# Kernel optimization log

Measured on AMD Instinct MI355X. Metric: run time of the kernel, lower is better.

## Reference

```python
import jax, jax.numpy as jnp
import numpy as np

BOS = 1
MAX_LEN = 20


def _lstm_cell(x, h, c, Wih, Whh, bih, bhh):
    # torch.nn.LSTMCell gate order: i, f, g, o
    g = x @ Wih.T + h @ Whh.T + bih + bhh
    i, f, gg, o = jnp.split(g, 4, axis=-1)
    c = jax.nn.sigmoid(f) * c + jax.nn.sigmoid(i) * jnp.tanh(gg)
    h = jax.nn.sigmoid(o) * jnp.tanh(c)
    return h, c


def setup_inputs() -> dict:
    key = jax.random.key(0)
    ks = jax.random.split(key, 12)
    B, K, D = 512, 36, 2048
    A, H, Em, V = 512, 512, 300, 10000
    s = 0.02
    rn = lambda k, shape, sc=s: sc * jax.random.normal(k, shape, dtype=jnp.float32)
    return {
        'feats': jax.random.normal(ks[0], (B, K, D), dtype=jnp.float32),
        'Wp': rn(ks[1], (A, D)), 'bp': jnp.zeros((A,), jnp.float32),
        'E': rn(ks[2], (V, Em), 0.1).at[0].set(0.0),  # padding_idx = 0
        'Wih1': rn(ks[3], (4 * H, Em + A)), 'Whh1': rn(ks[4], (4 * H, H)),
        'bih1': jnp.zeros((4 * H,), jnp.float32), 'bhh1': jnp.zeros((4 * H,), jnp.float32),
        'Wih2': rn(ks[5], (4 * H, H + A)), 'Whh2': rn(ks[6], (4 * H, H)),
        'bih2': jnp.zeros((4 * H,), jnp.float32), 'bhh2': jnp.zeros((4 * H,), jnp.float32),
        'Wa1': rn(ks[7], (A, H + A)), 'ba1': jnp.zeros((A,), jnp.float32),
        'wa2': rn(ks[8], (1, A)), 'ba2': jnp.zeros((1,), jnp.float32),
        'Wo': rn(ks[9], (V, H)), 'bo': jnp.zeros((V,), jnp.float32),
    }


def reference(feats, Wp, bp, E, Wih1, Whh1, bih1, bhh1, Wih2, Whh2, bih2, bhh2,
              Wa1, ba1, wa2, ba2, Wo, bo):
    B, K, D = feats.shape
    H = Whh1.shape[1]
    f_att = feats @ Wp.T + bp                      # [B, K, A]
    f_mean = f_att.mean(axis=1)                    # [B, A]
    # attn Linear over concat([h1, f_att]): split columns, precompute f_att term
    Wa1_h, Wa1_f = Wa1[:, :H], Wa1[:, H:]
    att_f = f_att @ Wa1_f.T + ba1                  # [B, K, A]
    x0 = jnp.broadcast_to(E[BOS], (B, E.shape[1]))
    z = jnp.zeros((B, H), jnp.float32)
    carry0 = (x0, z, z, z, z)

    def step(carry, _):
        x, h1, c1, h2, c2 = carry
        h1, c1 = _lstm_cell(jnp.concatenate([x, f_mean], axis=-1), h1, c1,
                            Wih1, Whh1, bih1, bhh1)
        pre = jnp.tanh(att_f + (h1 @ Wa1_h.T)[:, None, :])   # [B, K, A]
        e = pre @ wa2[0] + ba2[0]                            # [B, K]
        alpha = jax.nn.softmax(e, axis=-1)
        ctx = jnp.einsum('bk,bka->ba', alpha, f_att)         # [B, A]
        h2, c2 = _lstm_cell(jnp.concatenate([h1, ctx], axis=-1), h2, c2,
                            Wih2, Whh2, bih2, bhh2)
        logit = h2 @ Wo.T + bo                               # [B, V]  (dropout is identity in eval)
        nxt = jnp.argmax(logit, axis=-1)
        return (E[nxt], h1, c1, h2, c2), nxt

    _, ids = jax.lax.scan(step, carry0, None, length=MAX_LEN - 1)
    return ids.T  # [B, MAX_LEN-1], matches torch.stack(out_ids, 1)
```

## Files before the change

kernel.cpp:

```cpp
#include <hip/hip_runtime.h>
#include <math.h>
#include <stdint.h>

constexpr int Bsz = 512, Kf = 36, Dd = 2048, Aa = 512, Hh = 512, Em = 300;
constexpr int Vv = 10000, TSTEPS = 19, BOS = 1;
constexpr int K1 = 832;
constexpr int K2 = 1536;
constexpr int VvP = 10112;
constexpr int NTL = VvP / 64;
constexpr float SPLIT_S  = 2048.0f;
constexpr float SPLIT_IS = 1.0f / 2048.0f;

#define CDIV(a,b) (((a)+(b)-1)/(b))

typedef _Float16 f16x8 __attribute__((ext_vector_type(8)));
typedef float    f32x4 __attribute__((ext_vector_type(4)));

typedef const unsigned int GU __attribute__((address_space(1)));
typedef unsigned int       LU __attribute__((address_space(3)));

__device__ __forceinline__ void gload16(const void* g, void* l) {
    __builtin_amdgcn_global_load_lds((GU*)g, (LU*)l, 16, 0, 0);
}

template<int N> __device__ __forceinline__ void wait_vm() {
    if constexpr (N == 0)       asm volatile("s_waitcnt vmcnt(0)" ::: "memory");
    else if constexpr (N == 4)  asm volatile("s_waitcnt vmcnt(4)" ::: "memory");
    else if constexpr (N == 6)  asm volatile("s_waitcnt vmcnt(6)" ::: "memory");
    else if constexpr (N == 8)  asm volatile("s_waitcnt vmcnt(8)" ::: "memory");
    else if constexpr (N == 12) asm volatile("s_waitcnt vmcnt(12)" ::: "memory");
    else if constexpr (N == 16) asm volatile("s_waitcnt vmcnt(16)" ::: "memory");
    else static_assert(N == 0, "unsupported vmcnt literal");
}
#define WAIT_LGKM asm volatile("s_waitcnt lgkmcnt(0)" ::: "memory")
#define SB0 __builtin_amdgcn_sched_barrier(0)
#define BAR __builtin_amdgcn_s_barrier()

__device__ __forceinline__ float sigm(float v) { return 1.0f / (1.0f + expf(-v)); }

__device__ __forceinline__ void wsplit(_Float16* __restrict__ hi, _Float16* __restrict__ lo,
                                       size_t idx, float v) {
    _Float16 h = (_Float16)v;
    hi[idx] = h;
    lo[idx] = (_Float16)((v - (float)h) * SPLIT_S);
}


template<int BM, int BN, int BK, int DEPTH, int WVM, bool AF32, bool SWZ, int OCC, int EPI, int PAD>
__global__ __launch_bounds__(256, OCC)
void gemm_sp(const float* __restrict__ Af,
             const _Float16* __restrict__ Ahi, const _Float16* __restrict__ Alo, int lda,
             const _Float16* __restrict__ Bhi, const _Float16* __restrict__ Blo, int ldb,
             float* __restrict__ C, int ldc, int N, int K,
             const float* __restrict__ bias1, const float* __restrict__ bias2,
             const float* __restrict__ addC, int gxn,
             float* __restrict__ cbuf,
             _Float16* __restrict__ d1h, _Float16* __restrict__ d1l, int ld1, int off1,
             _Float16* __restrict__ d2h, _Float16* __restrict__ d2l, int ld2, int off2,
             float* __restrict__ candV, int* __restrict__ candI, int ntl)
{
    static_assert(EPI != 2 || WVM == 4, "LSTM epilogue needs 4x1 wave grid");
    constexpr int WVN = 4 / WVM;
    constexpr int WM = BM / WVM, WN = BN / WVN;
    constexpr int MF = WM / 16, NF = WN / 16;
    constexpr int PA  = BK / 8;
    constexpr int PSA = BM * 8 + PAD;
    constexpr int PSB = BN * 8 + PAD;
    static_assert(PAD == 0 || (BM >= 64 && BN >= 64), "PAD needs wave-aligned planes");
    constexpr int SZA = PA * PSA, SZB = PA * PSB;
    constexpr int OAH = 0, OAL = SZA, OBH = 2 * SZA, OBL = 2 * SZA + SZB;
    constexpr int BUF = 2 * SZA + 2 * SZB;
    constexpr int NCHA = BM * BK / 2048;
    constexpr int NCHB = BN * BK / 2048;
    static_assert(NCHA >= 1 && NCHB >= 1, "tile too small for 256-thread stage");
    constexpr int LW = 2 * NCHA + 2 * NCHB;
    static_assert((DEPTH & (DEPTH - 1)) == 0, "DEPTH pow2");
    static_assert(!AF32 || DEPTH == 2, "AF32 path is double-buffered");
    __shared__ _Float16 sm[DEPTH * BUF];

    int mt, nt;
    if constexpr (SWZ) {
        const int nwg = gridDim.x;
        const int cpx = nwg >> 3;
        const int orig = blockIdx.x;
        const int lid = (orig & 7) * cpx + (orig >> 3);
        nt = lid % gxn; mt = lid / gxn;
    } else {
        nt = blockIdx.x; mt = blockIdx.y;
    }
    const int m0 = mt * BM, n0 = nt * BN;

    const int t    = threadIdx.x;
    const int lane = t & 63;
    const int w    = t >> 6;
    const int wr   = w / WVN, wc = w % WVN;
    const int l15  = lane & 15, l4 = lane >> 4;

    f32x4 acch[MF][NF];
    f32x4 accm[MF][NF];
    #pragma unroll
    for (int m = 0; m < MF; ++m)
        #pragma unroll
        for (int n = 0; n < NF; ++n) {
            acch[m][n] = (f32x4){0.f, 0.f, 0.f, 0.f};
            accm[m][n] = (f32x4){0.f, 0.f, 0.f, 0.f};
        }

    const int nkt = K / BK;

    auto stageB = [&](int bufo, int kt) {
        #pragma unroll
        for (int i = 0; i < NCHB; ++i) {
            const int q  = i * 256 + t;
            const int p  = q / BN, r = q % BN;
            const int qw = i * 256 + (t & ~63);
            const int pu = qw / BN, ru = qw % BN;
            const size_t goff = (size_t)(n0 + r) * ldb + kt * BK + p * 8;
            gload16(Bhi + goff, &sm[bufo + OBH + pu * PSB + ru * 8]);
            gload16(Blo + goff, &sm[bufo + OBL + pu * PSB + ru * 8]);
        }
    };
    auto stageA16 = [&](int bufo, int kt) {
        #pragma unroll
        for (int i = 0; i < NCHA; ++i) {
            const int q  = i * 256 + t;
            const int p  = q / BM, r = q % BM;
            const int qw = i * 256 + (t & ~63);
            const int pu = qw / BM, ru = qw % BM;
            const size_t goff = (size_t)(m0 + r) * lda + kt * BK + p * 8;
            gload16(Ahi + goff, &sm[bufo + OAH + pu * PSA + ru * 8]);
            gload16(Alo + goff, &sm[bufo + OAL + pu * PSA + ru * 8]);
        }
    };
    auto issueA = [&](float4 (&rd)[NCHA][2], int kt) {
        #pragma unroll
        for (int i = 0; i < NCHA; ++i) {
            const int q = i * 256 + t;
            const int p = q / BM, r = q % BM;
            const float* src = Af + (size_t)(m0 + r) * lda + kt * BK + p * 8;
            rd[i][0] = *(const float4*)src;
            rd[i][1] = *(const float4*)(src + 4);
        }
    };
    auto writeA = [&](int bufo, float4 (&rd)[NCHA][2]) {
        #pragma unroll
        for (int i = 0; i < NCHA; ++i) {
            const int q = i * 256 + t;
            const int p = q / BM, r = q % BM;
            const float f[8] = {rd[i][0].x, rd[i][0].y, rd[i][0].z, rd[i][0].w,
                                rd[i][1].x, rd[i][1].y, rd[i][1].z, rd[i][1].w};
            f16x8 hi, lo;
            #pragma unroll
            for (int j = 0; j < 8; ++j) {
                _Float16 h = (_Float16)f[j];
                hi[j] = h;
                lo[j] = (_Float16)((f[j] - (float)h) * SPLIT_S);
            }
            *(f16x8*)&sm[bufo + OAH + p * PSA + r * 8] = hi;
            *(f16x8*)&sm[bufo + OAL + p * PSA + r * 8] = lo;
        }
    };
    auto compute = [&](int bufo) {
        #pragma unroll
        for (int s = 0; s < BK / 32; ++s) {
            f16x8 ah[MF], al[MF], bh[NF], bl[NF];
            const int pl = s * 4 + l4;
            #pragma unroll
            for (int m = 0; m < MF; ++m) {
                const int row = wr * WM + m * 16 + l15;
                ah[m] = *(const f16x8*)&sm[bufo + OAH + pl * PSA + row * 8];
                al[m] = *(const f16x8*)&sm[bufo + OAL + pl * PSA + row * 8];
            }
            #pragma unroll
            for (int n = 0; n < NF; ++n) {
                const int row = wc * WN + n * 16 + l15;
                bh[n] = *(const f16x8*)&sm[bufo + OBH + pl * PSB + row * 8];
                bl[n] = *(const f16x8*)&sm[bufo + OBL + pl * PSB + row * 8];
            }
            #pragma unroll
            for (int m = 0; m < MF; ++m)
                #pragma unroll
                for (int n = 0; n < NF; ++n) {
                    acch[m][n] = __builtin_amdgcn_mfma_f32_16x16x32_f16(ah[m], bh[n], acch[m][n], 0, 0, 0);
                    accm[m][n] = __builtin_amdgcn_mfma_f32_16x16x32_f16(ah[m], bl[n], accm[m][n], 0, 0, 0);
                    accm[m][n] = __builtin_amdgcn_mfma_f32_16x16x32_f16(al[m], bh[n], accm[m][n], 0, 0, 0);
                }
        }
    };

    if constexpr (AF32) {
        float4 rA[NCHA][2], rB[NCHA][2];
        issueA(rA, 0); stageB(0, 0);
        for (int kt = 0; kt < nkt; kt += 2) {
            issueA(rB, kt + 1); stageB(BUF, kt + 1);
            wait_vm<LW>(); SB0;
            writeA(0, rA);
            WAIT_LGKM; SB0;
            BAR; SB0;
            compute(0);
            SB0; WAIT_LGKM; BAR; SB0;
            if (kt + 2 < nkt) { issueA(rA, kt + 2); stageB(0, kt + 2); wait_vm<LW>(); }
            else              { wait_vm<0>(); }
            SB0;
            writeA(BUF, rB);
            WAIT_LGKM; SB0;
            BAR; SB0;
            compute(BUF);
            SB0; WAIT_LGKM; BAR; SB0;
        }
    } else {
        #pragma unroll
        for (int d = 0; d < DEPTH - 1; ++d) { stageA16(d * BUF, d); stageB(d * BUF, d); }
        for (int kt = 0; kt < nkt; ++kt) {
            const int bc = (kt & (DEPTH - 1)) * BUF;
            if (kt + DEPTH - 1 < nkt) {
                const int bn = ((kt + DEPTH - 1) & (DEPTH - 1)) * BUF;
                stageA16(bn, kt + DEPTH - 1); stageB(bn, kt + DEPTH - 1);
                wait_vm<(DEPTH - 1) * LW>();
            } else {
                const int rem = nkt - 1 - kt;
                if constexpr (DEPTH >= 4) {
                    if (rem >= 2)      wait_vm<2 * LW>();
                    else if (rem == 1) wait_vm<LW>();
                    else               wait_vm<0>();
                } else {
                    if (rem >= 1) wait_vm<LW>(); else wait_vm<0>();
                }
            }
            SB0;
            BAR; SB0;
            compute(bc);
            SB0; WAIT_LGKM; BAR; SB0;
        }
    }

    if constexpr (EPI == 0 || EPI == 1) {
        #pragma unroll
        for (int m = 0; m < MF; ++m) {
            const int rowb = m0 + wr * WM + m * 16 + l4 * 4;
            #pragma unroll
            for (int n = 0; n < NF; ++n) {
                const int col = n0 + wc * WN + n * 16 + l15;
                if (col < N) {
                    float bb = 0.f;
                    if (bias1) {
                        int bx = col;
                        if constexpr (EPI == 1)
                            bx = ((col & 63) >> 4) * 512 + ((col >> 6) << 4) + (col & 15);
                        bb += bias1[bx];
                        if (bias2) bb += bias2[bx];
                    }
                    #pragma unroll
                    for (int r = 0; r < 4; ++r) {
                        const size_t idx = (size_t)(rowb + r) * ldc + col;
                        float v = acch[m][n][r] + accm[m][n][r] * SPLIT_IS + bb;
                        if (addC) v += addC[idx];
                        C[idx] = v;
                    }
                }
            }
        }
    } else if constexpr (EPI == 2) {
        const int hh = (n0 >> 2) + l15;
        #pragma unroll
        for (int r = 0; r < 4; ++r) {
            const int row = m0 + wr * 16 + l4 * 4 + r;
            float v[4];
            #pragma unroll
            for (int n = 0; n < 4; ++n) {
                const int col = n0 + n * 16 + l15;
                float bb = 0.f;
                if (bias1) {
                    const int bx = ((col & 63) >> 4) * 512 + ((col >> 6) << 4) + (col & 15);
                    bb = bias1[bx] + bias2[bx];
                }
                float x = acch[0][n][r] + accm[0][n][r] * SPLIT_IS + bb;
                if (addC) x += addC[(size_t)row * ldc + col];
                v[n] = x;
            }
            const float cold = cbuf[(size_t)row * Hh + hh];
            const float cv = sigm(v[1]) * cold + sigm(v[0]) * tanhf(v[2]);
            cbuf[(size_t)row * Hh + hh] = cv;
            const float hv = sigm(v[3]) * tanhf(cv);
            wsplit(d1h, d1l, (size_t)row * ld1 + off1 + hh, hv);
            if (d2h) wsplit(d2h, d2l, (size_t)row * ld2 + off2 + hh, hv);
        }
    } else {
        float* sEv = reinterpret_cast<float*>(&sm[0]);
        int*   sEi = reinterpret_cast<int*>(&sm[0]) + 2 * BM;
        float bv[MF][4];
        int   bix[MF][4];
        #pragma unroll
        for (int m = 0; m < MF; ++m)
            #pragma unroll
            for (int r = 0; r < 4; ++r) { bv[m][r] = -INFINITY; bix[m][r] = 0x7fffffff; }
        #pragma unroll
        for (int m = 0; m < MF; ++m)
            #pragma unroll
            for (int r = 0; r < 4; ++r)
                #pragma unroll
                for (int n = 0; n < NF; ++n) {
                    const int col = n0 + wc * WN + n * 16 + l15;
                    if (col < N) {
                        const float x = acch[m][n][r] + accm[m][n][r] * SPLIT_IS + bias1[col];
                        if (x > bv[m][r]) { bv[m][r] = x; bix[m][r] = col; }
                    }
                }
        #pragma unroll
        for (int mask = 1; mask < 16; mask <<= 1) {
            #pragma unroll
            for (int m = 0; m < MF; ++m)
                #pragma unroll
                for (int r = 0; r < 4; ++r) {
                    const float ov = __shfl_xor(bv[m][r], mask);
                    const int   oi = __shfl_xor(bix[m][r], mask);
                    if (ov > bv[m][r] || (ov == bv[m][r] && oi < bix[m][r])) {
                        bv[m][r] = ov; bix[m][r] = oi;
                    }
                }
        }
        __syncthreads();
        if (l15 == 0) {
            #pragma unroll
            for (int m = 0; m < MF; ++m)
                #pragma unroll
                for (int r = 0; r < 4; ++r) {
                    const int rl = wr * WM + m * 16 + l4 * 4 + r;
                    sEv[wc * BM + rl] = bv[m][r];
                    sEi[wc * BM + rl] = bix[m][r];
                }
        }
        __syncthreads();
        if (t < BM) {
            float v0 = sEv[t]; int i0 = sEi[t];
            const float v1 = sEv[BM + t]; const int i1 = sEi[BM + t];
            if (v1 > v0 || (v1 == v0 && i1 < i0)) { v0 = v1; i0 = i1; }
            candV[(size_t)(m0 + t) * ntl + nt] = v0;
            candI[(size_t)(m0 + t) * ntl + nt] = i0;
        }
    }
}

__global__ __launch_bounds__(256)
void split_convert(const float* __restrict__ src, int srcld, int validR,
                   _Float16* __restrict__ dhi, _Float16* __restrict__ dlo,
                   int dstld, int coloff, int R, int C, int gperm)
{
    const int total = R * C;
    for (int i = blockIdx.x * 256 + threadIdx.x; i < total; i += gridDim.x * 256) {
        const int r = i / C, c = i % C;
        int dr = r;
        if (gperm) {
            const int gate = r >> 9, h = r & 511;
            dr = ((h >> 4) << 6) + (gate << 4) + (h & 15);
        }
        const float v = (r < validR) ? src[(size_t)r * srcld + c] : 0.f;
        wsplit(dhi, dlo, (size_t)dr * dstld + coloff + c, v);
    }
}

__global__ __launch_bounds__(256)
void init_kernel(_Float16* __restrict__ a1h0, _Float16* __restrict__ a1l0,
                 _Float16* __restrict__ a1h1, _Float16* __restrict__ a1l1,
                 _Float16* __restrict__ a2h0, _Float16* __restrict__ a2l0,
                 _Float16* __restrict__ a2h1, _Float16* __restrict__ a2l1,
                 float* __restrict__ c1, float* __restrict__ c2,
                 const float* __restrict__ E)
{
    const int idx = blockIdx.x * 256 + threadIdx.x;
    if (idx < Bsz * K1) {
        const int col = idx % K1;
        const float v = (col < Em) ? E[(size_t)BOS * Em + col] : 0.f;
        wsplit(a1h0, a1l0, idx, v);
        wsplit(a1h1, a1l1, idx, 0.f);
    }
    if (idx < Bsz * K2) {
        wsplit(a2h0, a2l0, idx, 0.f);
        wsplit(a2h1, a2l1, idx, 0.f);
    }
    if (idx < Bsz * Hh) { c1[idx] = 0.f; c2[idx] = 0.f; }
}

__global__ __launch_bounds__(256)
void fmean_kernel(const float* __restrict__ f_att, float* __restrict__ f_mean,
                  _Float16* __restrict__ fmh, _Float16* __restrict__ fml)
{
    const int b = blockIdx.x;
    for (int a = threadIdx.x; a < Aa; a += 256) {
        float s = 0.f;
        for (int k = 0; k < Kf; ++k) s += f_att[((size_t)b * Kf + k) * Aa + a];
        const float v = s * (1.0f / 36.0f);
        f_mean[(size_t)b * Aa + a] = v;
        wsplit(fmh, fml, (size_t)b * Aa + a, v);
    }
}

__global__ __launch_bounds__(256)
void attn_fused(const float* __restrict__ att_f, const float* __restrict__ q,
                const float* __restrict__ wa2, const float* __restrict__ ba2,
                const float* __restrict__ f_att,
                _Float16* __restrict__ a2h, _Float16* __restrict__ a2l)
{
    const int b = blockIdx.x, tid = threadIdx.x;
    const int w = tid >> 6, lane = tid & 63;
    __shared__ float se[Kf];
    __shared__ float wk[Kf];
    const float* pq = q + (size_t)b * Aa;
    for (int k = w; k < Kf; k += 4) {
        const float* pf = att_f + ((size_t)b * Kf + k) * Aa;
        float s = 0.f;
        #pragma unroll
        for (int j = 0; j < Aa; j += 64) {
            const int a = j + lane;
            s += tanhf(pf[a] + pq[a]) * wa2[a];
        }
        #pragma unroll
        for (int off = 32; off; off >>= 1) s += __shfl_down(s, off);
        if (lane == 0) se[k] = s + ba2[0];
    }
    __syncthreads();
    if (tid < Kf) {
        float mx = -INFINITY;
        for (int k = 0; k < Kf; ++k) mx = fmaxf(mx, se[k]);
        float ssum = 0.f;
        for (int k = 0; k < Kf; ++k) ssum += expf(se[k] - mx);
        wk[tid] = expf(se[tid] - mx) / ssum;
    }
    __syncthreads();
    for (int a = tid; a < Aa; a += 256) {
        float acc = 0.f;
        for (int k = 0; k < Kf; ++k)
            acc = fmaf(wk[k], f_att[((size_t)b * Kf + k) * Aa + a], acc);
        wsplit(a2h, a2l, (size_t)b * K2 + Hh + a, acc);
    }
}

__global__ __launch_bounds__(256)
void argmax_embed_kernel(const float* __restrict__ candV, const int* __restrict__ candI,
                         const float* __restrict__ E,
                         _Float16* __restrict__ a1h, _Float16* __restrict__ a1l,
                         int* __restrict__ out, int t, int ntl)
{
    const int b = blockIdx.x;
    const int tid = threadIdx.x;
    __shared__ float sv[256];
    __shared__ int   si[256];
    float bvv = -INFINITY; int bii = 0x7fffffff;
    if (tid < ntl) { bvv = candV[(size_t)b * ntl + tid]; bii = candI[(size_t)b * ntl + tid]; }
    sv[tid] = bvv; si[tid] = bii;
    __syncthreads();
    for (int s = 128; s > 0; s >>= 1) {
        if (tid < s) {
            const float v2 = sv[tid + s];
            const int   i2 = si[tid + s];
            if (v2 > sv[tid] || (v2 == sv[tid] && i2 < si[tid])) { sv[tid] = v2; si[tid] = i2; }
        }
        __syncthreads();
    }
    const int idx = si[0];
    if (tid == 0) out[(size_t)b * TSTEPS + t] = idx;
    for (int d = tid; d < Em; d += 256)
        wsplit(a1h, a1l, (size_t)b * K1 + d, E[(size_t)idx * Em + d]);
}

static inline void conv(hipStream_t s, const float* src, int srcld, int validR,
                        _Float16* dhi, _Float16* dlo, int dstld, int coloff,
                        int R, int C, int gperm)
{
    int blocks = CDIV(R * C, 256); if (blocks > 2048) blocks = 2048;
    split_convert<<<dim3(blocks), dim3(256), 0, s>>>(src, srcld, validR, dhi, dlo,
                                                     dstld, coloff, R, C, gperm);
}

extern "C" void kernel_launch(void* const* d_in, const int* in_sizes, int n_in,
                              void* d_out, int out_size, void* d_ws, size_t ws_size,
                              hipStream_t stream)
{
    const float* feats = (const float*)d_in[0];
    const float* Wp    = (const float*)d_in[1];
    const float* bp    = (const float*)d_in[2];
    const float* E     = (const float*)d_in[3];
    const float* Wih1  = (const float*)d_in[4];
    const float* Whh1  = (const float*)d_in[5];
    const float* bih1  = (const float*)d_in[6];
    const float* bhh1  = (const float*)d_in[7];
    const float* Wih2  = (const float*)d_in[8];
    const float* Whh2  = (const float*)d_in[9];
    const float* bih2  = (const float*)d_in[10];
    const float* bhh2  = (const float*)d_in[11];
    const float* Wa1   = (const float*)d_in[12];
    const float* ba1   = (const float*)d_in[13];
    const float* wa2   = (const float*)d_in[14];
    const float* ba2   = (const float*)d_in[15];
    const float* Wo    = (const float*)d_in[16];
    const float* bo    = (const float*)d_in[17];
    int* out = (int*)d_out;
    (void)in_sizes; (void)n_in; (void)out_size; (void)ws_size;

    uint8_t* w = (uint8_t*)d_ws;
    size_t off = 0;
    auto alloc = [&](size_t bytes) { void* p = w + off; off = (off + bytes + 255) & ~(size_t)255; return p; };

    float*     f_att  = (float*)alloc(18432ull * 512 * 4);
    float*     att_f  = (float*)alloc(18432ull * 512 * 4);
    float*     f_mean = (float*)alloc(512ull * 512 * 4);
    _Float16*  fmh    = (_Float16*)alloc(512ull * 512 * 2);
    _Float16*  fml    = (_Float16*)alloc(512ull * 512 * 2);
    _Float16*  wph    = (_Float16*)alloc(512ull * 2048 * 2);
    _Float16*  wpl    = (_Float16*)alloc(512ull * 2048 * 2);
    _Float16*  w1ph   = (_Float16*)alloc(2048ull * K1 * 2);
    _Float16*  w1pl   = (_Float16*)alloc(2048ull * K1 * 2);
    _Float16*  w1ch   = (_Float16*)alloc(2048ull * 512 * 2);
    _Float16*  w1cl   = (_Float16*)alloc(2048ull * 512 * 2);
    _Float16*  w2ph   = (_Float16*)alloc(2048ull * K2 * 2);
    _Float16*  w2pl   = (_Float16*)alloc(2048ull * K2 * 2);
    _Float16*  wahh   = (_Float16*)alloc(512ull * 512 * 2);
    _Float16*  wahl   = (_Float16*)alloc(512ull * 512 * 2);
    _Float16*  wafh   = (_Float16*)alloc(512ull * 512 * 2);
    _Float16*  wafl   = (_Float16*)alloc(512ull * 512 * 2);
    _Float16*  woh    = (_Float16*)alloc((size_t)VvP * 512 * 2);
    _Float16*  wol    = (_Float16*)alloc((size_t)VvP * 512 * 2);
    float*     g1c    = (float*)alloc(512ull * 2048 * 4);
    _Float16*  a1h[2] = {(_Float16*)alloc(512ull * K1 * 2), (_Float16*)alloc(512ull * K1 * 2)};
    _Float16*  a1l[2] = {(_Float16*)alloc(512ull * K1 * 2), (_Float16*)alloc(512ull * K1 * 2)};
    _Float16*  a2h[2] = {(_Float16*)alloc(512ull * K2 * 2), (_Float16*)alloc(512ull * K2 * 2)};
    _Float16*  a2l[2] = {(_Float16*)alloc(512ull * K2 * 2), (_Float16*)alloc(512ull * K2 * 2)};
    float*     c1     = (float*)alloc(512ull * 512 * 4);
    float*     c2     = (float*)alloc(512ull * 512 * 4);
    float*     qbuf   = (float*)alloc(512ull * 512 * 4);
    float*     candV  = (float*)alloc(512ull * NTL * 4);
    int*       candI  = (int*)alloc(512ull * NTL * 4);

    conv(stream, Wp,        Dd,      512,  wph,  wpl,  2048, 0,    512,  2048, 0);
    conv(stream, Wih1,      Em + Aa, 2048, w1ph, w1pl, K1,   0,    2048, Em,   1);
    conv(stream, Whh1,      Hh,      2048, w1ph, w1pl, K1,   Em,   2048, 512,  1);
    conv(stream, Wih1,      Em + Aa, 0,    w1ph, w1pl, K1,   812,  2048, 20,   0);
    conv(stream, Wih1 + Em, Em + Aa, 2048, w1ch, w1cl, 512,  0,    2048, 512,  1);
    conv(stream, Wih2,      Hh + Aa, 2048, w2ph, w2pl, K2,   0,    2048, 1024, 1);
    conv(stream, Whh2,      Hh,      2048, w2ph, w2pl, K2,   1024, 2048, 512,  1);
    conv(stream, Wa1,       Hh + Aa, 512,  wahh, wahl, 512,  0,    512,  512,  0);
    conv(stream, Wa1 + Hh,  Hh + Aa, 512,  wafh, wafl, 512,  0,    512,  512,  0);
    conv(stream, Wo,        Hh,      Vv,   woh,  wol,  512,  0,    VvP,  512,  0);

    init_kernel<<<dim3(CDIV(Bsz * K2, 256)), dim3(256), 0, stream>>>(
        a1h[0], a1l[0], a1h[1], a1l[1], a2h[0], a2l[0], a2h[1], a2l[1], c1, c2, E);

    gemm_sp<128, 64, 32, 2, 2, true, true, 2, 0, 8><<<dim3(1152), 256, 0, stream>>>(
        feats, nullptr, nullptr, Dd, wph, wpl, 2048, f_att, 512, 512, 2048,
        bp, nullptr, nullptr, 8,
        nullptr, nullptr, nullptr, 0, 0, nullptr, nullptr, 0, 0, nullptr, nullptr, 0);
    fmean_kernel<<<dim3(Bsz), dim3(256), 0, stream>>>(f_att, f_mean, fmh, fml);
    gemm_sp<64, 64, 64, 2, 2, false, false, 1, 1, 8><<<dim3(32, 8), 256, 0, stream>>>(
        nullptr, fmh, fml, 512, w1ch, w1cl, 512, g1c, 2048, 2048, 512,
        bih1, bhh1, nullptr, 0,
        nullptr, nullptr, nullptr, 0, 0, nullptr, nullptr, 0, 0, nullptr, nullptr, 0);
    gemm_sp<128, 64, 32, 2, 2, true, true, 2, 0, 8><<<dim3(1152), 256, 0, stream>>>(
        f_att, nullptr, nullptr, 512, wafh, wafl, 512, att_f, 512, 512, 512,
        ba1, nullptr, nullptr, 8,
        nullptr, nullptr, nullptr, 0, 0, nullptr, nullptr, 0, 0, nullptr, nullptr, 0);

    for (int t = 0; t < TSTEPS; ++t) {
        const int cur = t & 1, nxt = cur ^ 1;
        gemm_sp<64, 64, 32, 2, 4, false, false, 3, 2, 8><<<dim3(32, 8), 256, 0, stream>>>(
            nullptr, a1h[cur], a1l[cur], K1, w1ph, w1pl, K1, nullptr, 2048, 2048, K1,
            nullptr, nullptr, g1c, 0,
            c1, a2h[cur], a2l[cur], K2, 0, a1h[nxt], a1l[nxt], K1, Em,
            nullptr, nullptr, 0);
        gemm_sp<64, 64, 64, 2, 2, false, false, 1, 0, 8><<<dim3(8, 8), 256, 0, stream>>>(
            nullptr, a2h[cur], a2l[cur], K2, wahh, wahl, 512, qbuf, 512, 512, 512,
            nullptr, nullptr, nullptr, 0,
            nullptr, nullptr, nullptr, 0, 0, nullptr, nullptr, 0, 0, nullptr, nullptr, 0);
        attn_fused<<<dim3(Bsz), dim3(256), 0, stream>>>(
            att_f, qbuf, wa2, ba2, f_att, a2h[cur], a2l[cur]);
        gemm_sp<64, 64, 32, 2, 4, false, false, 3, 2, 8><<<dim3(32, 8), 256, 0, stream>>>(
            nullptr, a2h[cur], a2l[cur], K2, w2ph, w2pl, K2, nullptr, 2048, 2048, K2,
            bih2, bhh2, nullptr, 0,
            c2, a2h[nxt], a2l[nxt], K2, 1024, nullptr, nullptr, 0, 0,
            nullptr, nullptr, 0);
        gemm_sp<64, 64, 64, 2, 2, false, false, 1, 3, 8><<<dim3(NTL, 8), 256, 0, stream>>>(
            nullptr, a2h[nxt] + 1024, a2l[nxt] + 1024, K2, woh, wol, 512, nullptr, 0, Vv, 512,
            bo, nullptr, nullptr, 0,
            nullptr, nullptr, nullptr, 0, 0, nullptr, nullptr, 0, 0, candV, candI, NTL);
        argmax_embed_kernel<<<dim3(Bsz), dim3(256), 0, stream>>>(
            candV, candI, E, a1h[nxt], a1l[nxt], out, t, NTL);
    }
}
```

Measured before the change: 3.542 ms.

## Split fp32-A GEMM into dedicated 512-thread kernel and raise LSTM GEMM BK to 64

```diff
diff --git a/kernel.cpp b/kernel.cpp
--- a/kernel.cpp
+++ b/kernel.cpp
@@ -25,11 +25,9 @@
 
 template<int N> __device__ __forceinline__ void wait_vm() {
     if constexpr (N == 0)       asm volatile("s_waitcnt vmcnt(0)" ::: "memory");
-    else if constexpr (N == 4)  asm volatile("s_waitcnt vmcnt(4)" ::: "memory");
+    else if constexpr (N == 3)  asm volatile("s_waitcnt vmcnt(3)" ::: "memory");
     else if constexpr (N == 6)  asm volatile("s_waitcnt vmcnt(6)" ::: "memory");
     else if constexpr (N == 8)  asm volatile("s_waitcnt vmcnt(8)" ::: "memory");
-    else if constexpr (N == 12) asm volatile("s_waitcnt vmcnt(12)" ::: "memory");
-    else if constexpr (N == 16) asm volatile("s_waitcnt vmcnt(16)" ::: "memory");
     else static_assert(N == 0, "unsupported vmcnt literal");
 }
 #define WAIT_LGKM asm volatile("s_waitcnt lgkmcnt(0)" ::: "memory")
@@ -46,14 +44,13 @@
 }
 
 
-template<int BM, int BN, int BK, int DEPTH, int WVM, bool AF32, bool SWZ, int OCC, int EPI, int PAD>
+template<int BM, int BN, int BK, int WVM, int OCC, int EPI>
 __global__ __launch_bounds__(256, OCC)
-void gemm_sp(const float* __restrict__ Af,
-             const _Float16* __restrict__ Ahi, const _Float16* __restrict__ Alo, int lda,
+void gemm_sp(const _Float16* __restrict__ Ahi, const _Float16* __restrict__ Alo, int lda,
              const _Float16* __restrict__ Bhi, const _Float16* __restrict__ Blo, int ldb,
              float* __restrict__ C, int ldc, int N, int K,
              const float* __restrict__ bias1, const float* __restrict__ bias2,
-             const float* __restrict__ addC, int gxn,
+             const float* __restrict__ addC,
              float* __restrict__ cbuf,
              _Float16* __restrict__ d1h, _Float16* __restrict__ d1l, int ld1, int off1,
              _Float16* __restrict__ d2h, _Float16* __restrict__ d2l, int ld2, int off2,
@@ -64,30 +61,17 @@
     constexpr int WM = BM / WVM, WN = BN / WVN;
     constexpr int MF = WM / 16, NF = WN / 16;
     constexpr int PA  = BK / 8;
-    constexpr int PSA = BM * 8 + PAD;
-    constexpr int PSB = BN * 8 + PAD;
-    static_assert(PAD == 0 || (BM >= 64 && BN >= 64), "PAD needs wave-aligned planes");
+    constexpr int PSA = BM * 8 + 8;
+    constexpr int PSB = BN * 8 + 8;
     constexpr int SZA = PA * PSA, SZB = PA * PSB;
     constexpr int OAH = 0, OAL = SZA, OBH = 2 * SZA, OBL = 2 * SZA + SZB;
     constexpr int BUF = 2 * SZA + 2 * SZB;
     constexpr int NCHA = BM * BK / 2048;
     constexpr int NCHB = BN * BK / 2048;
-    static_assert(NCHA >= 1 && NCHB >= 1, "tile too small for 256-thread stage");
     constexpr int LW = 2 * NCHA + 2 * NCHB;
-    static_assert((DEPTH & (DEPTH - 1)) == 0, "DEPTH pow2");
-    static_assert(!AF32 || DEPTH == 2, "AF32 path is double-buffered");
-    __shared__ _Float16 sm[DEPTH * BUF];
-
-    int mt, nt;
-    if constexpr (SWZ) {
-        const int nwg = gridDim.x;
-        const int cpx = nwg >> 3;
-        const int orig = blockIdx.x;
-        const int lid = (orig & 7) * cpx + (orig >> 3);
-        nt = lid % gxn; mt = lid / gxn;
-    } else {
-        nt = blockIdx.x; mt = blockIdx.y;
-    }
+    __shared__ _Float16 sm[2 * BUF];
+
+    const int nt = blockIdx.x, mt = blockIdx.y;
     const int m0 = mt * BM, n0 = nt * BN;
 
     const int t    = threadIdx.x;
@@ -108,7 +92,17 @@
 
     const int nkt = K / BK;
 
-    auto stageB = [&](int bufo, int kt) {
+    auto stage = [&](int bufo, int kt) {
+        #pragma unroll
+        for (int i = 0; i < NCHA; ++i) {
+            const int q  = i * 256 + t;
+            const int p  = q / BM, r = q % BM;
+            const int qw = i * 256 + (t & ~63);
+            const int pu = qw / BM, ru = qw % BM;
+            const size_t goff = (size_t)(m0 + r) * lda + kt * BK + p * 8;
+            gload16(Ahi + goff, &sm[bufo + OAH + pu * PSA + ru * 8]);
+            gload16(Alo + goff, &sm[bufo + OAL + pu * PSA + ru * 8]);
+        }
         #pragma unroll
         for (int i = 0; i < NCHB; ++i) {
             const int q  = i * 256 + t;
@@ -120,46 +114,6 @@
             gload16(Blo + goff, &sm[bufo + OBL + pu * PSB + ru * 8]);
         }
     };
-    auto stageA16 = [&](int bufo, int kt) {
-        #pragma unroll
-        for (int i = 0; i < NCHA; ++i) {
-            const int q  = i * 256 + t;
-            const int p  = q / BM, r = q % BM;
-            const int qw = i * 256 + (t & ~63);
-            const int pu = qw / BM, ru = qw % BM;
-            const size_t goff = (size_t)(m0 + r) * lda + kt * BK + p * 8;
-            gload16(Ahi + goff, &sm[bufo + OAH + pu * PSA + ru * 8]);
-            gload16(Alo + goff, &sm[bufo + OAL + pu * PSA + ru * 8]);
-        }
-    };
-    auto issueA = [&](float4 (&rd)[NCHA][2], int kt) {
-        #pragma unroll
-        for (int i = 0; i < NCHA; ++i) {
-            const int q = i * 256 + t;
-            const int p = q / BM, r = q % BM;
-            const float* src = Af + (size_t)(m0 + r) * lda + kt * BK + p * 8;
-            rd[i][0] = *(const float4*)src;
-            rd[i][1] = *(const float4*)(src + 4);
-        }
-    };
-    auto writeA = [&](int bufo, float4 (&rd)[NCHA][2]) {
-        #pragma unroll
-        for (int i = 0; i < NCHA; ++i) {
-            const int q = i * 256 + t;
-            const int p = q / BM, r = q % BM;
-            const float f[8] = {rd[i][0].x, rd[i][0].y, rd[i][0].z, rd[i][0].w,
-                                rd[i][1].x, rd[i][1].y, rd[i][1].z, rd[i][1].w};
-            f16x8 hi, lo;
-            #pragma unroll
-            for (int j = 0; j < 8; ++j) {
-                _Float16 h = (_Float16)f[j];
-                hi[j] = h;
-                lo[j] = (_Float16)((f[j] - (float)h) * SPLIT_S);
-            }
-            *(f16x8*)&sm[bufo + OAH + p * PSA + r * 8] = hi;
-            *(f16x8*)&sm[bufo + OAL + p * PSA + r * 8] = lo;
-        }
-    };
     auto compute = [&](int bufo) {
         #pragma unroll
         for (int s = 0; s < BK / 32; ++s) {
@@ -188,50 +142,15 @@
         }
     };
 
-    if constexpr (AF32) {
-        float4 rA[NCHA][2], rB[NCHA][2];
-        issueA(rA, 0); stageB(0, 0);
-        for (int kt = 0; kt < nkt; kt += 2) {
-            issueA(rB, kt + 1); stageB(BUF, kt + 1);
-            wait_vm<LW>(); SB0;
-            writeA(0, rA);
-            WAIT_LGKM; SB0;
-            BAR; SB0;
-            compute(0);
-            SB0; WAIT_LGKM; BAR; SB0;
-            if (kt + 2 < nkt) { issueA(rA, kt + 2); stageB(0, kt + 2); wait_vm<LW>(); }
-            else              { wait_vm<0>(); }
-            SB0;
-            writeA(BUF, rB);
-            WAIT_LGKM; SB0;
-            BAR; SB0;
-            compute(BUF);
-            SB0; WAIT_LGKM; BAR; SB0;
-        }
-    } else {
-        #pragma unroll
-        for (int d = 0; d < DEPTH - 1; ++d) { stageA16(d * BUF, d); stageB(d * BUF, d); }
-        for (int kt = 0; kt < nkt; ++kt) {
-            const int bc = (kt & (DEPTH - 1)) * BUF;
-            if (kt + DEPTH - 1 < nkt) {
-                const int bn = ((kt + DEPTH - 1) & (DEPTH - 1)) * BUF;
-                stageA16(bn, kt + DEPTH - 1); stageB(bn, kt + DEPTH - 1);
-                wait_vm<(DEPTH - 1) * LW>();
-            } else {
-                const int rem = nkt - 1 - kt;
-                if constexpr (DEPTH >= 4) {
-                    if (rem >= 2)      wait_vm<2 * LW>();
-                    else if (rem == 1) wait_vm<LW>();
-                    else               wait_vm<0>();
-                } else {
-                    if (rem >= 1) wait_vm<LW>(); else wait_vm<0>();
-                }
-            }
-            SB0;
-            BAR; SB0;
-            compute(bc);
-            SB0; WAIT_LGKM; BAR; SB0;
-        }
+    stage(0, 0);
+    for (int kt = 0; kt < nkt; ++kt) {
+        const int bc = (kt & 1) * BUF;
+        if (kt + 1 < nkt) { stage(BUF - bc, kt + 1); wait_vm<LW>(); }
+        else              { wait_vm<0>(); }
+        SB0;
+        BAR; SB0;
+        compute(bc);
+        SB0; WAIT_LGKM; BAR; SB0;
     }
 
     if constexpr (EPI == 0 || EPI == 1) {
@@ -337,6 +256,136 @@
             if (v1 > v0 || (v1 == v0 && i1 < i0)) { v0 = v1; i0 = i1; }
             candV[(size_t)(m0 + t) * ntl + nt] = v0;
             candI[(size_t)(m0 + t) * ntl + nt] = i0;
+        }
+    }
+}
+
+__global__ __launch_bounds__(512, 4)
+void gemm_af32(const float* __restrict__ Af, int lda,
+               const _Float16* __restrict__ Bhi, const _Float16* __restrict__ Blo, int ldb,
+               float* __restrict__ C, int ldc, int N, int K,
+               const float* __restrict__ bias1, int gxn)
+{
+    constexpr int BM = 128, BN = 64, BK = 32;
+    constexpr int WM = 32, WN = 32;
+    constexpr int MF = 2, NF = 2;
+    constexpr int PSA = BM * 8 + 8;
+    constexpr int PSB = BN * 8 + 8;
+    constexpr int PA  = BK / 8;
+    constexpr int SZA = PA * PSA, SZB = PA * PSB;
+    constexpr int OAH = 0, OAL = SZA, OBH = 2 * SZA, OBL = 2 * SZA + SZB;
+    constexpr int BUF = 2 * SZA + 2 * SZB;
+    __shared__ _Float16 sm[2 * BUF];
+
+    const int nwg = gridDim.x;
+    const int cpx = nwg >> 3;
+    const int orig = blockIdx.x;
+    const int lid = (orig & 7) * cpx + (orig >> 3);
+    const int nt = lid % gxn, mt = lid / gxn;
+    const int m0 = mt * BM, n0 = nt * BN;
+
+    const int t    = threadIdx.x;
+    const int lane = t & 63;
+    const int w    = t >> 6;
+    const int wr   = w >> 1, wc = w & 1;
+    const int l15  = lane & 15, l4 = lane >> 4;
+    const int ar   = t >> 2, ac = t & 3;
+
+    f32x4 acch[MF][NF];
+    f32x4 accm[MF][NF];
+    #pragma unroll
+    for (int m = 0; m < MF; ++m)
+        #pragma unroll
+        for (int n = 0; n < NF; ++n) {
+            acch[m][n] = (f32x4){0.f, 0.f, 0.f, 0.f};
+            accm[m][n] = (f32x4){0.f, 0.f, 0.f, 0.f};
+        }
+
+    const int nkt = K / BK;
+
+    auto issueA = [&](float4 (&rd)[2], int kt) {
+        const float* src = Af + (size_t)(m0 + ar) * lda + kt * BK + ac * 8;
+        rd[0] = *(const float4*)src;
+        rd[1] = *(const float4*)(src + 4);
+    };
+    auto writeA = [&](int bufo, float4 (&rd)[2]) {
+        const float f[8] = {rd[0].x, rd[0].y, rd[0].z, rd[0].w,
+                            rd[1].x, rd[1].y, rd[1].z, rd[1].w};
+        f16x8 hi, lo;
+        #pragma unroll
+        for (int j = 0; j < 8; ++j) {
+            _Float16 h = (_Float16)f[j];
+            hi[j] = h;
+            lo[j] = (_Float16)((f[j] - (float)h) * SPLIT_S);
+        }
+        *(f16x8*)&sm[bufo + OAH + ac * PSA + ar * 8] = hi;
+        *(f16x8*)&sm[bufo + OAL + ac * PSA + ar * 8] = lo;
+    };
+    auto stageB = [&](int bufo, int kt) {
+        const int q = t & 255;
+        const int p = q >> 6, r = q & 63;
+        const _Float16* src = (t < 256) ? Bhi : Blo;
+        const int base = (t < 256) ? (bufo + OBH) : (bufo + OBL);
+        const size_t goff = (size_t)(n0 + r) * ldb + kt * BK + p * 8;
+        gload16(src + goff, &sm[base + p * PSB + r * 8]);
+    };
+    auto compute = [&](int bufo) {
+        f16x8 ah[MF], al[MF], bh[NF], bl[NF];
+        const int pl = l4;
+        #pragma unroll
+        for (int m = 0; m < MF; ++m) {
+            const int row = wr * WM + m * 16 + l15;
+            ah[m] = *(const f16x8*)&sm[bufo + OAH + pl * PSA + row * 8];
+            al[m] = *(const f16x8*)&sm[bufo + OAL + pl * PSA + row * 8];
+        }
+        #pragma unroll
+        for (int n = 0; n < NF; ++n) {
+            const int row = wc * WN + n * 16 + l15;
+            bh[n] = *(const f16x8*)&sm[bufo + OBH + pl * PSB + row * 8];
+            bl[n] = *(const f16x8*)&sm[bufo + OBL + pl * PSB + row * 8];
+        }
+        #pragma unroll
+        for (int m = 0; m < MF; ++m)
+            #pragma unroll
+            for (int n = 0; n < NF; ++n) {
+                acch[m][n] = __builtin_amdgcn_mfma_f32_16x16x32_f16(ah[m], bh[n], acch[m][n], 0, 0, 0);
+                accm[m][n] = __builtin_amdgcn_mfma_f32_16x16x32_f16(ah[m], bl[n], accm[m][n], 0, 0, 0);
+                accm[m][n] = __builtin_amdgcn_mfma_f32_16x16x32_f16(al[m], bh[n], accm[m][n], 0, 0, 0);
+            }
+    };
+
+    float4 rA[2], rB[2];
+    issueA(rA, 0); stageB(0, 0);
+    for (int kt = 0; kt < nkt; kt += 2) {
+        issueA(rB, kt + 1); stageB(BUF, kt + 1);
+        wait_vm<3>(); SB0;
+        writeA(0, rA);
+        WAIT_LGKM; SB0;
+        BAR; SB0;
+        compute(0);
+        SB0; WAIT_LGKM; BAR; SB0;
+        if (kt + 2 < nkt) { issueA(rA, kt + 2); stageB(0, kt + 2); wait_vm<3>(); }
+        else              { wait_vm<0>(); }
+        SB0;
+        writeA(BUF, rB);
+        WAIT_LGKM; SB0;
+        BAR; SB0;
+        compute(BUF);
+        SB0; WAIT_LGKM; BAR; SB0;
+    }
+
+    #pragma unroll
+    for (int m = 0; m < MF; ++m) {
+        const int rowb = m0 + wr * WM + m * 16 + l4 * 4;
+        #pragma unroll
+        for (int n = 0; n < NF; ++n) {
+            const int col = n0 + wc * WN + n * 16 + l15;
+            float bb = bias1 ? bias1[col] : 0.f;
+            #pragma unroll
+            for (int r = 0; r < 4; ++r) {
+                const size_t idx = (size_t)(rowb + r) * ldc + col;
+                C[idx] = acch[m][n][r] + accm[m][n][r] * SPLIT_IS + bb;
+            }
         }
     }
 }
@@ -534,7 +583,7 @@
     conv(stream, Wp,        Dd,      512,  wph,  wpl,  2048, 0,    512,  2048, 0);
     conv(stream, Wih1,      Em + Aa, 2048, w1ph, w1pl, K1,   0,    2048, Em,   1);
     conv(stream, Whh1,      Hh,      2048, w1ph, w1pl, K1,   Em,   2048, 512,  1);
-    conv(stream, Wih1,      Em + Aa, 0,    w1ph, w1pl, K1,   812,  2048, 20,   0);
+    conv(stream, Wih1,      Em + Aa, 0,    w1ph, w1pl, K1,   812,  2048, 20,   1);
     conv(stream, Wih1 + Em, Em + Aa, 2048, w1ch, w1cl, 512,  0,    2048, 512,  1);
     conv(stream, Wih2,      Hh + Aa, 2048, w2ph, w2pl, K2,   0,    2048, 1024, 1);
     conv(stream, Whh2,      Hh,      2048, w2ph, w2pl, K2,   1024, 2048, 512,  1);
@@ -545,41 +594,37 @@
     init_kernel<<<dim3(CDIV(Bsz * K2, 256)), dim3(256), 0, stream>>>(
         a1h[0], a1l[0], a1h[1], a1l[1], a2h[0], a2l[0], a2h[1], a2l[1], c1, c2, E);
 
-    gemm_sp<128, 64, 32, 2, 2, true, true, 2, 0, 8><<<dim3(1152), 256, 0, stream>>>(
-        feats, nullptr, nullptr, Dd, wph, wpl, 2048, f_att, 512, 512, 2048,
-        bp, nullptr, nullptr, 8,
+    gemm_af32<<<dim3(1152), dim3(512), 0, stream>>>(
+        feats, Dd, wph, wpl, 2048, f_att, 512, 512, 2048, bp, 8);
+    fmean_kernel<<<dim3(Bsz), dim3(256), 0, stream>>>(f_att, f_mean, fmh, fml);
+    gemm_sp<64, 64, 64, 2, 1, 1><<<dim3(32, 8), 256, 0, stream>>>(
+        fmh, fml, 512, w1ch, w1cl, 512, g1c, 2048, 2048, 512,
+        bih1, bhh1, nullptr,
         nullptr, nullptr, nullptr, 0, 0, nullptr, nullptr, 0, 0, nullptr, nullptr, 0);
-    fmean_kernel<<<dim3(Bsz), dim3(256), 0, stream>>>(f_att, f_mean, fmh, fml);
-    gemm_sp<64, 64, 64, 2, 2, false, false, 1, 1, 8><<<dim3(32, 8), 256, 0, stream>>>(
-        nullptr, fmh, fml, 512, w1ch, w1cl, 512, g1c, 2048, 2048, 512,
-        bih1, bhh1, nullptr, 0,
-        nullptr, nullptr, nullptr, 0, 0, nullptr, nullptr, 0, 0, nullptr, nullptr, 0);
-    gemm_sp<128, 64, 32, 2, 2, true, true, 2, 0, 8><<<dim3(1152), 256, 0, stream>>>(
-        f_att, nullptr, nullptr, 512, wafh, wafl, 512, att_f, 512, 512, 512,
-        ba1, nullptr, nullptr, 8,
-        nullptr, nullptr, nullptr, 0, 0, nullptr, nullptr, 0, 0, nullptr, nullptr, 0);
+    gemm_af32<<<dim3(1152), dim3(512), 0, stream>>>(
+        f_att, 512, wafh, wafl, 512, att_f, 512, 512, 512, ba1, 8);
 
     for (int t = 0; t < TSTEPS; ++t) {
         const int cur = t & 1, nxt = cur ^ 1;
-        gemm_sp<64, 64, 32, 2, 4, false, false, 3, 2, 8><<<dim3(32, 8), 256, 0, stream>>>(
-            nullptr, a1h[cur], a1l[cur], K1, w1ph, w1pl, K1, nullptr, 2048, 2048, K1,
-            nullptr, nullptr, g1c, 0,
+        gemm_sp<64, 64, 64, 4, 2, 2><<<dim3(32, 8), 256, 0, stream>>>(
+            a1h[cur], a1l[cur], K1, w1ph, w1pl, K1, nullptr, 2048, 2048, K1,
+            nullptr, nullptr, g1c,
             c1, a2h[cur], a2l[cur], K2, 0, a1h[nxt], a1l[nxt], K1, Em,
             nullptr, nullptr, 0);
-        gemm_sp<64, 64, 64, 2, 2, false, false, 1, 0, 8><<<dim3(8, 8), 256, 0, stream>>>(
-            nullptr, a2h[cur], a2l[cur], K2, wahh, wahl, 512, qbuf, 512, 512, 512,
-            nullptr, nullptr, nullptr, 0,
+        gemm_sp<64, 64, 64, 2, 1, 0><<<dim3(8, 8), 256, 0, stream>>>(
+            a2h[cur], a2l[cur], K2, wahh, wahl, 512, qbuf, 512, 512, 512,
+            nullptr, nullptr, nullptr,
             nullptr, nullptr, nullptr, 0, 0, nullptr, nullptr, 0, 0, nullptr, nullptr, 0);
         attn_fused<<<dim3(Bsz), dim3(256), 0, stream>>>(
             att_f, qbuf, wa2, ba2, f_att, a2h[cur], a2l[cur]);
-        gemm_sp<64, 64, 32, 2, 4, false, false, 3, 2, 8><<<dim3(32, 8), 256, 0, stream>>>(
-            nullptr, a2h[cur], a2l[cur], K2, w2ph, w2pl, K2, nullptr, 2048, 2048, K2,
-            bih2, bhh2, nullptr, 0,
+        gemm_sp<64, 64, 64, 4, 2, 2><<<dim3(32, 8), 256, 0, stream>>>(
+            a2h[cur], a2l[cur], K2, w2ph, w2pl, K2, nullptr, 2048, 2048, K2,
+            bih2, bhh2, nullptr,
             c2, a2h[nxt], a2l[nxt], K2, 1024, nullptr, nullptr, 0, 0,
             nullptr, nullptr, 0);
-        gemm_sp<64, 64, 64, 2, 2, false, false, 1, 3, 8><<<dim3(NTL, 8), 256, 0, stream>>>(
-            nullptr, a2h[nxt] + 1024, a2l[nxt] + 1024, K2, woh, wol, 512, nullptr, 0, Vv, 512,
-            bo, nullptr, nullptr, 0,
+        gemm_sp<64, 64, 64, 2, 1, 3><<<dim3(NTL, 8), 256, 0, stream>>>(
+            a2h[nxt] + 1024, a2l[nxt] + 1024, K2, woh, wol, 512, nullptr, 0, Vv, 512,
+            bo, nullptr, nullptr,
             nullptr, nullptr, nullptr, 0, 0, nullptr, nullptr, 0, 0, candV, candI, NTL);
         argmax_embed_kernel<<<dim3(Bsz), dim3(256), 0, stream>>>(
             candV, candI, E, a1h[nxt], a1l[nxt], out, t, NTL);
```

Result: faster. 3.394 ms, median of 3 (-4.2%).
